# Kernel optimization log

Measured on AMD Instinct MI355X. Metric: run time of the kernel, lower is better.

## Reference

```python
import jax, jax.numpy as jnp
import numpy as np

B, N, D, H, DH, FF, CI, K, MPE = 8, 1024, 512, 8, 64, 2048, 1024, 31, 512
PAD = (K // 2, K // 2 - (K + 1) % 2)  # (15, 15)


def _ln(x, g, b):
    m = x.mean(-1, keepdims=True)
    v = ((x - m) ** 2).mean(-1, keepdims=True)
    return (x - m) * jax.lax.rsqrt(v + 1e-5) * g + b


def _swish(x):
    return x * jax.nn.sigmoid(x)


def setup_inputs() -> dict:
    key = jax.random.key(0)
    ks = iter(jax.random.split(key, 40))
    def w(shape, s=0.02):
        return (jax.random.normal(next(ks), shape) * s).astype(jnp.float32)
    ones = lambda n: jnp.ones((n,), jnp.float32)
    zeros = lambda n: jnp.zeros((n,), jnp.float32)
    return dict(
        x=jax.random.normal(next(ks), (B, N, D), dtype=jnp.float32),
        f1_g=ones(D), f1_b=zeros(D), f1_w1=w((D, FF)), f1_b1=zeros(FF), f1_w2=w((FF, D)), f1_b2=zeros(D),
        a_g=ones(D), a_b=zeros(D), wq=w((D, H * DH)), wkv=w((D, 2 * H * DH)), wo=w((H * DH, D)), wo_b=zeros(D),
        rel=w((2 * MPE + 1, DH)),
        c_g=ones(D), c_b=zeros(D), cw1=w((D, 2 * CI)), cb1=zeros(2 * CI), dw=w((CI, K)), db=zeros(CI),
        bn_g=ones(CI), bn_b=zeros(CI), bn_m=zeros(CI), bn_v=ones(CI), cw2=w((CI, D)), cb2=zeros(D),
        f2_g=ones(D), f2_b=zeros(D), f2_w1=w((D, FF)), f2_b1=zeros(FF), f2_w2=w((FF, D)), f2_b2=zeros(D),
        p_g=ones(D), p_b=zeros(D),
    )


def reference(x, f1_g, f1_b, f1_w1, f1_b1, f1_w2, f1_b2,
              a_g, a_b, wq, wkv, wo, wo_b, rel,
              c_g, c_b, cw1, cb1, dw, db, bn_g, bn_b, bn_m, bn_v, cw2, cb2,
              f2_g, f2_b, f2_w1, f2_b1, f2_w2, f2_b2, p_g, p_b):
    # FF1 (half-step)
    h = _ln(x, f1_g, f1_b)
    x = x + 0.5 * (_swish(h @ f1_w1 + f1_b1) @ f1_w2 + f1_b2)
    # Attention with relative positional bias
    h = _ln(x, a_g, a_b)
    q = (h @ wq).reshape(B, N, H, DH).transpose(0, 2, 1, 3)          # bhnd
    k, v = jnp.split(h @ wkv, 2, axis=-1)
    k = k.reshape(B, N, H, DH).transpose(0, 2, 1, 3)
    v = v.reshape(B, N, H, DH).transpose(0, 2, 1, 3)
    scale = DH ** -0.5
    dots = jnp.einsum('bhid,bhjd->bhij', q, k) * scale
    seq = jnp.arange(N)
    dist = jnp.clip(seq[:, None] - seq[None, :], -MPE, MPE) + MPE    # [N,N]
    rp = rel[dist]                                                   # [N,N,DH]
    dots = dots + jnp.einsum('bhnd,nrd->bhnr', q, rp) * scale
    attn = jax.nn.softmax(dots, axis=-1)
    o = jnp.einsum('bhij,bhjd->bhid', attn, v).transpose(0, 2, 1, 3).reshape(B, N, H * DH)
    x = x + o @ wo + wo_b
    # Conv module: LN -> pw conv -> GLU -> depthwise conv -> BN(eval) -> swish -> pw conv
    h = _ln(x, c_g, c_b)
    h = h @ cw1 + cb1                                                # [B,N,2CI]
    out, gate = jnp.split(h, 2, axis=-1)
    h = (out * jax.nn.sigmoid(gate)).transpose(0, 2, 1)              # [B,CI,N]
    h = jnp.pad(h, ((0, 0), (0, 0), PAD))
    h = jax.lax.conv_general_dilated(h, dw[:, None, :], (1,), 'VALID',
                                     feature_group_count=CI,
                                     dimension_numbers=('NCH', 'OIH', 'NCH')) + db[None, :, None]
    h = (h - bn_m[None, :, None]) * jax.lax.rsqrt(bn_v[None, :, None] + 1e-5) * bn_g[None, :, None] + bn_b[None, :, None]
    h = _swish(h).transpose(0, 2, 1)                                 # [B,N,CI]
    x = x + h @ cw2 + cb2
    # FF2 (half-step) + post norm
    h = _ln(x, f2_g, f2_b)
    x = x + 0.5 * (_swish(h @ f2_w1 + f2_b1) @ f2_w2 + f2_b2)
    return _ln(x, p_g, p_b)
```

## Files before the change

kernel.cpp:

```cpp
#include <hip/hip_runtime.h>
#include <hip/hip_bf16.h>
#include <cstdint>


using bf16_t = __hip_bfloat16;
typedef __bf16 bf16x8 __attribute__((ext_vector_type(8)));
typedef float floatx4 __attribute__((ext_vector_type(4)));

struct alignas(16) hbf8 { bf16_t h[8]; };
struct alignas(8)  hbf4 { bf16_t h[4]; };

__device__ __forceinline__ float  b2f(bf16_t h) { return __bfloat162float(h); }
__device__ __forceinline__ bf16_t f2b(float f)  { return __float2bfloat16(f); }
__device__ __forceinline__ float  sig_(float x) { return 1.f / (1.f + __expf(-x)); }

__device__ __forceinline__ void async16(const void* g, void* l) {
  __builtin_amdgcn_global_load_lds(
      (const __attribute__((address_space(1))) unsigned int*)(uintptr_t)g,
      (__attribute__((address_space(3))) unsigned int*)(uintptr_t)l, 16, 0, 0);
}

struct GemmArgs {
  const bf16_t* A; const bf16_t* Bt; const float* bias; const float* srcf;
  bf16_t* C; float* resid;
  int K, lda, ldb, ldc;
  long sAb, sAh, sBb, sBh, sCb, sCh;
  float alpha, beta;
};

template <int BM, int BN, int WR, int WC, int EPI>
__global__ __launch_bounds__(256) void gemm_bt(GemmArgs g) {
  constexpr int FM = BM / (WR * 16);
  constexpr int FN = BN / (WC * 16);
  constexpr int IA = (BM * 4) / 256;
  constexpr int IB = (BN * 4) / 256;
  __shared__ __align__(16) bf16_t As[BM * 32];
  __shared__ __align__(16) bf16_t Bs[BN * 32];
  const int tid = threadIdx.x;
  const int lane = tid & 63, w = tid >> 6;
  int bx = blockIdx.x, by = blockIdx.y;
  {
    const int gx = gridDim.x;
    const int nwg = gx * gridDim.y;
    if ((nwg & 7) == 0 && gridDim.z == 1) {
      int lin = by * gx + bx;
      int lid = (lin & 7) * (nwg >> 3) + (lin >> 3);
      bx = lid % gx; by = lid / gx;
    }
  }
  const int bm0 = by * BM, bn0 = bx * BN;
  const int zb = blockIdx.z >> 3, zh = blockIdx.z & 7;
  const bf16_t* Ab = g.A + (long)zb * g.sAb + (long)zh * g.sAh;
  const bf16_t* Bb = g.Bt + (long)zb * g.sBb + (long)zh * g.sBh;
  const int wm0 = (w / WC) * (FM * 16);
  const int wn0 = (w % WC) * (FN * 16);
  const int lrow = lane & 15, lq = lane >> 4;

  floatx4 acc[FM][FN] = {};

  for (int k0 = 0; k0 < g.K; k0 += 32) {
#pragma unroll
    for (int i = 0; i < IA; ++i) {
      int c = i * 256 + tid;
      int m = c >> 2, kk = (c & 3) * 8;
      async16(Ab + (long)(bm0 + m) * g.lda + (k0 + kk), (char*)As + c * 16);
    }
#pragma unroll
    for (int i = 0; i < IB; ++i) {
      int c = i * 256 + tid;
      int n = bn0 + (c >> 2), kk = (c & 3) * 8;
      async16(Bb + (long)n * g.ldb + (k0 + kk), (char*)Bs + c * 16);
    }
    __syncthreads();
    bf16x8 af[FM], bfr[FN];
#pragma unroll
    for (int fm = 0; fm < FM; ++fm)
      af[fm] = *(const bf16x8*)(As + (wm0 + fm * 16 + lrow) * 32 + lq * 8);
#pragma unroll
    for (int fn = 0; fn < FN; ++fn)
      bfr[fn] = *(const bf16x8*)(Bs + (wn0 + fn * 16 + lrow) * 32 + lq * 8);
#pragma unroll
    for (int fm = 0; fm < FM; ++fm)
#pragma unroll
      for (int fn = 0; fn < FN; ++fn)
        acc[fm][fn] = __builtin_amdgcn_mfma_f32_16x16x32_bf16(af[fm], bfr[fn], acc[fm][fn], 0, 0, 0);
    __syncthreads();
  }

  const int bi = bm0 + wm0 + lq * 4;
  const int bj = bn0 + wn0 + lrow;
  if constexpr (EPI == 2) {
    float* R = g.resid;
    const float* S = g.srcf;
#pragma unroll
    for (int fm = 0; fm < FM; ++fm)
#pragma unroll
      for (int fn = 0; fn < FN; ++fn) {
        int j = bj + fn * 16;
        float bv = g.bias ? g.bias[j] : 0.f;
#pragma unroll
        for (int r = 0; r < 4; ++r) {
          long i = bi + fm * 16 + r;
          float base = S ? S[i * g.ldc + j] : R[i * g.ldc + j];
          R[i * g.ldc + j] = base + g.beta * (acc[fm][fn][r] + bv);
        }
      }
  } else if constexpr (EPI == 4) {
    bf16_t* C = g.C;
#pragma unroll
    for (int fm = 0; fm < FM; ++fm)
#pragma unroll
      for (int fn = 0; fn < FN; ++fn) {
        int j = bj + fn * 16;
        float bv = g.bias[(j >> 1) + (j & 1) * 1024];
#pragma unroll
        for (int r = 0; r < 4; ++r) {
          int i = bi + fm * 16 + r;
          float v = acc[fm][fn][r] + bv;
          float gp = __shfl_xor(v, 1);
          if ((j & 1) == 0)
            C[(long)i * g.ldc + (j >> 1)] = f2b(v * sig_(gp));
        }
      }
  } else {
    bf16_t* C = g.C + (long)zb * g.sCb + (long)zh * g.sCh;
#pragma unroll
    for (int fm = 0; fm < FM; ++fm)
#pragma unroll
      for (int fn = 0; fn < FN; ++fn) {
        int j = bj + fn * 16;
        float bv = g.bias ? g.bias[j] : 0.f;
#pragma unroll
        for (int r = 0; r < 4; ++r) {
          int i = bi + fm * 16 + r;
          float v = acc[fm][fn][r];
          if constexpr (EPI == 0) v = g.alpha * v + bv;
          if constexpr (EPI == 1) { v += bv; v = v * sig_(v); }
          C[(long)i * g.ldc + j] = f2b(v);
        }
      }
  }
}

__global__ __launch_bounds__(512, 4) void attn_kernel(
    const bf16_t* __restrict__ QKV, const bf16_t* __restrict__ VT,
    const bf16_t* __restrict__ RELP, bf16_t* __restrict__ O) {
  constexpr int LDT = 1028;
  __shared__ __align__(16) bf16_t Tls[32 * LDT];
  __shared__ float scr[576];

  const int tid = threadIdx.x;
  const int w = tid >> 6, lane = tid & 63;
  const int lrow = lane & 15, lq = lane >> 4;
  const int lin = blockIdx.y * gridDim.x + blockIdx.x;
  const int lid = (lin & 7) * 256 + (lin >> 3);
  const int z = lid >> 5;
  const int i0 = (lid & 31) * 32;
  const int b = z >> 3, zh = z & 7;
  const int j0w = w * 128;

  const bf16_t* Qb  = QKV + ((long)(b * 1024 + i0)) * 1536 + zh * 64;
  const bf16_t* Kb  = QKV + ((long)b * 1024) * 1536 + 512 + zh * 64;
  const bf16_t* VTb = VT + ((long)(b * 8 + zh)) * 65536;

  bf16x8 af[2][2];
#pragma unroll
  for (int fm = 0; fm < 2; ++fm)
#pragma unroll
    for (int ks = 0; ks < 2; ++ks)
      af[fm][ks] = *(const bf16x8*)(Qb + (long)(fm * 16 + lrow) * 1536 + ks * 32 + lq * 8);

  {
    const int u0w = w * 144;
    bf16x8 rf[18];
#pragma unroll
    for (int fnT = 0; fnT < 9; ++fnT) {
      const int u0 = u0w + fnT * 16;
      if (u0 < LDT) {
        rf[2 * fnT]     = *(const bf16x8*)(RELP + (long)(u0 + lrow) * 64 + lq * 8);
        rf[2 * fnT + 1] = *(const bf16x8*)(RELP + (long)(u0 + lrow) * 64 + 32 + lq * 8);
      }
    }
#pragma unroll
    for (int fnT = 0; fnT < 9; ++fnT) {
      const int u0 = u0w + fnT * 16;
      if (u0 < LDT) {
        floatx4 tacc[2] = {};
        tacc[0] = __builtin_amdgcn_mfma_f32_16x16x32_bf16(af[0][0], rf[2 * fnT],     tacc[0], 0, 0, 0);
        tacc[0] = __builtin_amdgcn_mfma_f32_16x16x32_bf16(af[0][1], rf[2 * fnT + 1], tacc[0], 0, 0, 0);
        tacc[1] = __builtin_amdgcn_mfma_f32_16x16x32_bf16(af[1][0], rf[2 * fnT],     tacc[1], 0, 0, 0);
        tacc[1] = __builtin_amdgcn_mfma_f32_16x16x32_bf16(af[1][1], rf[2 * fnT + 1], tacc[1], 0, 0, 0);
        const int uu = u0 + lrow;
#pragma unroll
        for (int fm = 0; fm < 2; ++fm)
#pragma unroll
          for (int r = 0; r < 4; ++r)
            if (uu < LDT)
              Tls[(fm * 16 + lq * 4 + r) * LDT + uu] = f2b(tacc[fm][r]);
      }
    }
  }

  bf16x8 kfA[8], kfB[8];
#pragma unroll
  for (int x = 0; x < 8; ++x)
    kfA[x] = *(const bf16x8*)(Kb + (long)(j0w + (x >> 1) * 16 + lrow) * 1536 + (x & 1) * 32 + lq * 8);
#pragma unroll
  for (int x = 0; x < 8; ++x)
    kfB[x] = *(const bf16x8*)(Kb + (long)(j0w + (4 + (x >> 1)) * 16 + lrow) * 1536 + (x & 1) * 32 + lq * 8);
  __syncthreads();

  floatx4 sacc[2][8] = {};
#pragma unroll
  for (int fn = 0; fn < 4; ++fn) {
    sacc[0][fn] = __builtin_amdgcn_mfma_f32_16x16x32_bf16(af[0][0], kfA[2 * fn],     sacc[0][fn], 0, 0, 0);
    sacc[0][fn] = __builtin_amdgcn_mfma_f32_16x16x32_bf16(af[0][1], kfA[2 * fn + 1], sacc[0][fn], 0, 0, 0);
    sacc[1][fn] = __builtin_amdgcn_mfma_f32_16x16x32_bf16(af[1][0], kfA[2 * fn],     sacc[1][fn], 0, 0, 0);
    sacc[1][fn] = __builtin_amdgcn_mfma_f32_16x16x32_bf16(af[1][1], kfA[2 * fn + 1], sacc[1][fn], 0, 0, 0);
  }
#pragma unroll
  for (int fn = 4; fn < 8; ++fn) {
    sacc[0][fn] = __builtin_amdgcn_mfma_f32_16x16x32_bf16(af[0][0], kfB[2 * (fn - 4)],     sacc[0][fn], 0, 0, 0);
    sacc[0][fn] = __builtin_amdgcn_mfma_f32_16x16x32_bf16(af[0][1], kfB[2 * (fn - 4) + 1], sacc[0][fn], 0, 0, 0);
    sacc[1][fn] = __builtin_amdgcn_mfma_f32_16x16x32_bf16(af[1][0], kfB[2 * (fn - 4)],     sacc[1][fn], 0, 0, 0);
    sacc[1][fn] = __builtin_amdgcn_mfma_f32_16x16x32_bf16(af[1][1], kfB[2 * (fn - 4) + 1], sacc[1][fn], 0, 0, 0);
  }

#pragma unroll
  for (int fm = 0; fm < 2; ++fm)
#pragma unroll
    for (int r = 0; r < 4; ++r) {
      const int il = fm * 16 + lq * 4 + r;
      const bf16_t* trow = Tls + il * LDT + 512;
      const int tb = i0 + il - j0w - lrow;
#pragma unroll
      for (int fn = 0; fn < 8; ++fn) {
        int t = tb - fn * 16;
        t = t < -512 ? -512 : (t > 512 ? 512 : t);
        sacc[fm][fn][r] += b2f(trow[t]);
      }
    }

  float rmax[2][4];
#pragma unroll
  for (int fm = 0; fm < 2; ++fm)
#pragma unroll
    for (int r = 0; r < 4; ++r) {
      float m = sacc[fm][0][r];
#pragma unroll
      for (int fn = 1; fn < 8; ++fn) m = fmaxf(m, sacc[fm][fn][r]);
      rmax[fm][r] = m;
    }
#pragma unroll
  for (int off = 1; off < 16; off <<= 1)
#pragma unroll
    for (int fm = 0; fm < 2; ++fm)
#pragma unroll
      for (int r = 0; r < 4; ++r)
        rmax[fm][r] = fmaxf(rmax[fm][r], __shfl_xor(rmax[fm][r], off));
  if (lrow == 0)
#pragma unroll
    for (int fm = 0; fm < 2; ++fm)
#pragma unroll
      for (int r = 0; r < 4; ++r)
        scr[(fm * 16 + lq * 4 + r) * 9 + w] = rmax[fm][r];

  float rsum[2][4];
#pragma unroll
  for (int fm = 0; fm < 2; ++fm)
#pragma unroll
    for (int r = 0; r < 4; ++r) {
      float s = 0.f;
#pragma unroll
      for (int fn = 0; fn < 8; ++fn) {
        float e = __expf(sacc[fm][fn][r] - rmax[fm][r]);
        sacc[fm][fn][r] = e;
        s += e;
      }
      rsum[fm][r] = s;
    }
#pragma unroll
  for (int off = 1; off < 16; off <<= 1)
#pragma unroll
    for (int fm = 0; fm < 2; ++fm)
#pragma unroll
      for (int r = 0; r < 4; ++r)
        rsum[fm][r] += __shfl_xor(rsum[fm][r], off);
  if (lrow == 0)
#pragma unroll
    for (int fm = 0; fm < 2; ++fm)
#pragma unroll
      for (int r = 0; r < 4; ++r)
        scr[288 + (fm * 16 + lq * 4 + r) * 9 + w] = rsum[fm][r];

  bf16x8 vfA[8];
#pragma unroll
  for (int x = 0; x < 8; ++x)
    vfA[x] = *(const bf16x8*)(VTb + (long)((x & 3) * 16 + lrow) * 1024 + j0w + (x >> 2) * 32 + lq * 8);

  __syncthreads();

#pragma unroll
  for (int fm = 0; fm < 2; ++fm)
#pragma unroll
    for (int fn = 0; fn < 8; ++fn)
#pragma unroll
      for (int r = 0; r < 4; ++r) {
        const int i = fm * 16 + lq * 4 + r;
        const int j = j0w + fn * 16 + lrow;
        const unsigned boff = (unsigned)(i * 2048 + j * 2) ^ ((unsigned)(i & 7) << 4);
        *(bf16_t*)((char*)Tls + boff) = f2b(sacc[fm][fn][r]);
      }

  bf16x8 vfB[8];
#pragma unroll
  for (int x = 0; x < 8; ++x)
    vfB[x] = *(const bf16x8*)(VTb + (long)((x & 3) * 16 + lrow) * 1024 + j0w + 64 + (x >> 2) * 32 + lq * 8);

  floatx4 oacc[2][4] = {};
#pragma unroll
  for (int ks = 0; ks < 4; ++ks) {
    const int j = j0w + ks * 32;
    bf16x8 ap[2];
#pragma unroll
    for (int fm = 0; fm < 2; ++fm) {
      const int i = fm * 16 + lrow;
      const unsigned boff = (unsigned)(i * 2048 + (j + lq * 8) * 2) ^ ((unsigned)(i & 7) << 4);
      ap[fm] = *(const bf16x8*)((char*)Tls + boff);
    }
#pragma unroll
    for (int fd = 0; fd < 4; ++fd) {
      bf16x8 bv = (ks < 2) ? vfA[(ks << 2) | fd] : vfB[((ks - 2) << 2) | fd];
      oacc[0][fd] = __builtin_amdgcn_mfma_f32_16x16x32_bf16(ap[0], bv, oacc[0][fd], 0, 0, 0);
      oacc[1][fd] = __builtin_amdgcn_mfma_f32_16x16x32_bf16(ap[1], bv, oacc[1][fd], 0, 0, 0);
    }
  }
  __syncthreads();

  {
    float* part = (float*)Tls + w * 2048;
#pragma unroll
    for (int fm = 0; fm < 2; ++fm)
#pragma unroll
      for (int fd = 0; fd < 4; ++fd)
#pragma unroll
        for (int r = 0; r < 4; ++r)
          part[(fm * 16 + lq * 4 + r) * 64 + fd * 16 + lrow] = oacc[fm][fd][r];
  }
  __syncthreads();

  {
    const int i = tid >> 4;
    const int d0 = (tid & 15) * 4;
    float mw[8], sw[8];
#pragma unroll
    for (int ww = 0; ww < 8; ++ww) {
      mw[ww] = scr[i * 9 + ww];
      sw[ww] = scr[288 + i * 9 + ww];
    }
    float M = mw[0];
#pragma unroll
    for (int ww = 1; ww < 8; ++ww) M = fmaxf(M, mw[ww]);
    float fac[8]; float tot = 0.f;
#pragma unroll
    for (int ww = 0; ww < 8; ++ww) { fac[ww] = __expf(mw[ww] - M); tot += sw[ww] * fac[ww]; }
    const float inv = 1.f / tot;
    floatx4 s = {};
#pragma unroll
    for (int ww = 0; ww < 8; ++ww) {
      floatx4 p = *(const floatx4*)((const float*)Tls + ww * 2048 + i * 64 + d0);
      s += p * fac[ww];
    }
    hbf4 o4;
#pragma unroll
    for (int m = 0; m < 4; ++m) o4.h[m] = f2b(s[m] * inv);
    *(hbf4*)(O + (long)(b * 1024 + i0 + i) * 512 + zh * 64 + d0) = o4;
  }
}

__global__ __launch_bounds__(256) void diag_kernel(float* __restrict__ out, long n, float v) {
  long i = (long)blockIdx.x * 256 + threadIdx.x;
  if (i < n) out[i] = v;
}

struct PrepJobs {
  const float* src[10];
  bf16_t*      dst[10];
  int R[10], C[10], gx[10], start[10];
  float scale[10];
  int   mode[10];
  int   njobs;
};

__global__ __launch_bounds__(256) void prep_kernel(PrepJobs P) {
  __shared__ float t[32][33];
  const int bid = blockIdx.x;
  int j = 0;
  while (j + 1 < P.njobs && bid >= P.start[j + 1]) ++j;
  const int tile = bid - P.start[j];
  const int tid = threadIdx.x;
  if (P.mode[j] == 2) {
    int i = tile * 256 + tid;
    if (i < 73728) {
      int r = i >> 6, c = i & 63;
      P.dst[j][i] = (r < 1025) ? f2b(P.src[j][r * 64 + c]) : f2b(0.f);
    }
    return;
  }
  const int gx = P.gx[j];
  const int c0 = (tile % gx) * 32, r0 = (tile / gx) * 32;
  const int C = P.C[j], R = P.R[j];
  const float scale = P.scale[j];
  const int tx = tid & 31, ty = tid >> 5;
#pragma unroll
  for (int i = 0; i < 4; ++i)
    t[ty + i * 8][tx] = P.src[j][(long)(r0 + ty + i * 8) * C + c0 + tx];
  __syncthreads();
#pragma unroll
  for (int i = 0; i < 4; ++i) {
    int c = c0 + ty + i * 8;
    int row = (P.mode[j] == 1) ? ((c < 1024) ? 2 * c : 2 * (c - 1024) + 1) : c;
    P.dst[j][(long)row * R + r0 + tx] = f2b(t[tx][ty + i * 8] * scale);
  }
}

template <bool F32OUT>
__global__ __launch_bounds__(256) void ln_kernel(const float* __restrict__ X, const float* __restrict__ gam,
                                                 const float* __restrict__ bet, void* __restrict__ outv) {
  int row = blockIdx.x, tid = threadIdx.x;
  const float* x = X + (long)row * 512;
  float a = x[tid], b = x[tid + 256];
  float s = a + b, q = a * a + b * b;
  for (int off = 32; off; off >>= 1) { s += __shfl_down(s, off); q += __shfl_down(q, off); }
  __shared__ float red[8];
  int w = tid >> 6;
  if ((tid & 63) == 0) { red[w] = s; red[w + 4] = q; }
  __syncthreads();
  float ts = red[0] + red[1] + red[2] + red[3];
  float tq = red[4] + red[5] + red[6] + red[7];
  float mean = ts * (1.f / 512.f);
  float var = tq * (1.f / 512.f) - mean * mean;
  float rs = rsqrtf(var + 1e-5f);
  float o0 = (a - mean) * rs * gam[tid]       + bet[tid];
  float o1 = (b - mean) * rs * gam[tid + 256] + bet[tid + 256];
  if constexpr (F32OUT) {
    float* out = (float*)outv;
    out[(long)row * 512 + tid]       = o0;
    out[(long)row * 512 + tid + 256] = o1;
  } else {
    bf16_t* out = (bf16_t*)outv;
    out[(long)row * 512 + tid]       = f2b(o0);
    out[(long)row * 512 + tid + 256] = f2b(o1);
  }
}

__global__ __launch_bounds__(256) void vt_kernel(const bf16_t* __restrict__ QKV, bf16_t* __restrict__ VT) {
  int jb = blockIdx.x, z = blockIdx.y;
  int b = z >> 3, h = z & 7;
  const bf16_t* src = QKV + (long)b * 1024 * 1536 + 1024 + h * 64;
  bf16_t* dst = VT + (long)z * 65536;
  __shared__ bf16_t t[64][65];
  int tid = threadIdx.x;
#pragma unroll
  for (int i = 0; i < 16; ++i) {
    int l = i * 256 + tid;
    int j = l >> 6, d = l & 63;
    t[d][j] = src[(long)(jb * 64 + j) * 1536 + d];
  }
  __syncthreads();
#pragma unroll
  for (int i = 0; i < 16; ++i) {
    int l = i * 256 + tid;
    int d = l >> 6, j = l & 63;
    dst[(long)d * 1024 + jb * 64 + j] = t[d][j];
  }
}

__global__ __launch_bounds__(256) void dwconv_kernel(const bf16_t* __restrict__ G, const float* __restrict__ dw,
    const float* __restrict__ db, const float* __restrict__ bng, const float* __restrict__ bnb,
    const float* __restrict__ bnm, const float* __restrict__ bnv, bf16_t* __restrict__ out) {
  int n0 = blockIdx.x * 32, c0 = blockIdx.y * 64, b = blockIdx.z;
  __shared__ bf16_t t[62][64];
  __shared__ float dws[31][64];
  int tid = threadIdx.x;
  const bf16_t* src = G + (long)b * 1024 * 1024 + c0;
#pragma unroll
  for (int i = 0; i < 16; ++i) {
    int l = i * 256 + tid;
    if (l < 3968) {
      int rr = l >> 6, c = l & 63;
      int n = n0 - 15 + rr;
      t[rr][c] = (n >= 0 && n < 1024) ? src[(long)n * 1024 + c] : f2b(0.f);
    }
  }
#pragma unroll
  for (int i = 0; i < 8; ++i) {
    int l = i * 256 + tid;
    if (l < 1984) {
      int k = l >> 6, c = l & 63;
      dws[k][c] = dw[(long)(c0 + c) * 31 + k];
    }
  }
  __syncthreads();
  int c = tid & 63, nl = tid >> 6;
  float rs = rsqrtf(bnv[c0 + c] + 1e-5f);
  float sc = rs * bng[c0 + c];
  float ab = (db[c0 + c] - bnm[c0 + c]) * sc + bnb[c0 + c];
#pragma unroll
  for (int j = 0; j < 8; ++j) {
    int rr = nl * 8 + j;
    float s = 0.f;
#pragma unroll
    for (int k = 0; k < 31; ++k) s += b2f(t[rr + k][c]) * dws[k][c];
    float y = s * sc + ab;
    out[((long)b * 1024 + n0 + rr) * 1024 + c0 + c] = f2b(y * sig_(y));
  }
}

extern "C" void kernel_launch(void* const* d_in, const int* in_sizes, int n_in,
                              void* d_out, int out_size, void* d_ws, size_t ws_size,
                              hipStream_t stream) {
  auto fail = [&](float code) {
    diag_kernel<<<(out_size + 255) / 256, 256, 0, stream>>>((float*)d_out, out_size, code);
  };
  if (n_in != 34)             { fail(70.f);  return; }
  if (in_sizes[0] != 4194304) { fail(80.f);  return; }

  const float* x     = (const float*)d_in[0];
  const float* f1_g  = (const float*)d_in[1];
  const float* f1_b  = (const float*)d_in[2];
  const float* f1_w1 = (const float*)d_in[3];
  const float* f1_b1 = (const float*)d_in[4];
  const float* f1_w2 = (const float*)d_in[5];
  const float* f1_b2 = (const float*)d_in[6];
  const float* a_g   = (const float*)d_in[7];
  const float* a_b   = (const float*)d_in[8];
  const float* wq    = (const float*)d_in[9];
  const float* wkv   = (const float*)d_in[10];
  const float* wo    = (const float*)d_in[11];
  const float* wo_b  = (const float*)d_in[12];
  const float* rel   = (const float*)d_in[13];
  const float* c_g   = (const float*)d_in[14];
  const float* c_b   = (const float*)d_in[15];
  const float* cw1   = (const float*)d_in[16];
  const float* cb1   = (const float*)d_in[17];
  const float* dwp   = (const float*)d_in[18];
  const float* dbp   = (const float*)d_in[19];
  const float* bn_g  = (const float*)d_in[20];
  const float* bn_b  = (const float*)d_in[21];
  const float* bn_m  = (const float*)d_in[22];
  const float* bn_v  = (const float*)d_in[23];
  const float* cw2   = (const float*)d_in[24];
  const float* cb2   = (const float*)d_in[25];
  const float* f2_g  = (const float*)d_in[26];
  const float* f2_b  = (const float*)d_in[27];
  const float* f2_w1 = (const float*)d_in[28];
  const float* f2_b1 = (const float*)d_in[29];
  const float* f2_w2 = (const float*)d_in[30];
  const float* f2_b2 = (const float*)d_in[31];
  const float* p_g   = (const float*)d_in[32];
  const float* p_b   = (const float*)d_in[33];

  char* ws = (char*)d_ws;
  const size_t OFF_X  = 0;
  const size_t OFF_WT = 16777216;
  const size_t OFF_D  = 30408704;
  const size_t OFF_E  = 63963136;
  const size_t relp_off = OFF_E + 33554432;
  if (ws_size < relp_off + 147456ULL) { fail(200.f); return; }

  float*  X   = (float*)(ws + OFF_X);
  bf16_t* WT  = (bf16_t*)(ws + OFF_WT);
  bf16_t* QKV = (bf16_t*)(ws + OFF_D);
  bf16_t* VT  = (bf16_t*)(ws + OFF_D + 25165824);
  bf16_t* GLU = (bf16_t*)(ws + OFF_D);
  bf16_t* DWO = (bf16_t*)(ws + OFF_D + 16777216);
  bf16_t* MID = (bf16_t*)(ws + OFF_E);
  bf16_t* RELP= (bf16_t*)(ws + relp_off);
  bf16_t* H   = (bf16_t*)d_out;
  bf16_t* O   = (bf16_t*)d_out;

  bf16_t* f1_w1t = WT;            bf16_t* f1_w2t = WT + 1048576;
  bf16_t* wqkvt  = WT + 2097152;
  bf16_t* wot    = WT + 2883584;  bf16_t* cw1t   = WT + 3145728;
  bf16_t* cw2t   = WT + 4194304;  bf16_t* f2_w1t = WT + 4718592;
  bf16_t* f2_w2t = WT + 5767168;

  auto GA = [](const bf16_t* A, const bf16_t* Bt, const float* bias, bf16_t* C,
               float* resid, const float* srcf, int K, int lda, int ldb, int ldc,
               float alpha, float beta) {
    GemmArgs g{}; g.A = A; g.Bt = Bt; g.bias = bias; g.srcf = srcf; g.C = C; g.resid = resid;
    g.K = K; g.lda = lda; g.ldb = ldb; g.ldc = ldc;
    g.sAb = g.sAh = g.sBb = g.sBh = g.sCb = g.sCh = 0; g.alpha = alpha; g.beta = beta;
    return g;
  };

  {
    PrepJobs P{};
    auto set = [&](int idx, const float* s, bf16_t* d, int R, int C, int start,
                   float sc, int mode) {
      P.src[idx] = s; P.dst[idx] = d; P.R[idx] = R; P.C[idx] = C;
      P.gx[idx] = C / 32; P.start[idx] = start; P.scale[idx] = sc; P.mode[idx] = mode;
    };
    set(0, f1_w1, f1_w1t,          512, 2048,    0, 1.f,    0);
    set(1, f1_w2, f1_w2t,         2048,  512, 1024, 1.f,    0);
    set(2, wq,    wqkvt,           512,  512, 2048, 0.125f, 0);
    set(3, wkv,   wqkvt + 262144,  512, 1024, 2304, 1.f,    0);
    set(4, wo,    wot,             512,  512, 2816, 1.f,    0);
    set(5, cw1,   cw1t,            512, 2048, 3072, 1.f,    1);
    set(6, cw2,   cw2t,           1024,  512, 4096, 1.f,    0);
    set(7, f2_w1, f2_w1t,          512, 2048, 4608, 1.f,    0);
    set(8, f2_w2, f2_w2t,         2048,  512, 5632, 1.f,    0);
    set(9, rel,   RELP,           1025,   64, 6656, 1.f,    2);
    P.njobs = 10;
    prep_kernel<<<6944, 256, 0, stream>>>(P);
  }

  ln_kernel<false><<<8192, 256, 0, stream>>>(x, f1_g, f1_b, H);
  { GemmArgs g = GA(H, f1_w1t, f1_b1, MID, nullptr, nullptr, 512, 512, 512, 2048, 1.f, 0.f);
    gemm_bt<128, 128, 2, 2, 1><<<dim3(16, 64, 1), 256, 0, stream>>>(g); }
  { GemmArgs g = GA(MID, f1_w2t, f1_b2, nullptr, X, x, 2048, 2048, 2048, 512, 1.f, 0.5f);
    gemm_bt<64, 128, 1, 4, 2><<<dim3(4, 128, 1), 256, 0, stream>>>(g); }

  ln_kernel<false><<<8192, 256, 0, stream>>>(X, a_g, a_b, H);
  { GemmArgs g = GA(H, wqkvt, nullptr, QKV, nullptr, nullptr, 512, 512, 512, 1536, 1.f, 0.f);
    gemm_bt<128, 128, 2, 2, 0><<<dim3(12, 64, 1), 256, 0, stream>>>(g); }
  vt_kernel<<<dim3(16, 64), 256, 0, stream>>>(QKV, VT);

  attn_kernel<<<dim3(32, 64), 512, 0, stream>>>(QKV, VT, RELP, O);

  { GemmArgs g = GA(O, wot, wo_b, nullptr, X, nullptr, 512, 512, 512, 512, 1.f, 1.f);
    gemm_bt<64, 128, 1, 4, 2><<<dim3(4, 128, 1), 256, 0, stream>>>(g); }

  ln_kernel<false><<<8192, 256, 0, stream>>>(X, c_g, c_b, H);
  { GemmArgs g = GA(H, cw1t, cb1, GLU, nullptr, nullptr, 512, 512, 512, 1024, 1.f, 0.f);
    gemm_bt<128, 128, 2, 2, 4><<<dim3(16, 64, 1), 256, 0, stream>>>(g); }
  dwconv_kernel<<<dim3(32, 16, 8), 256, 0, stream>>>(GLU, dwp, dbp, bn_g, bn_b, bn_m, bn_v, DWO);
  { GemmArgs g = GA(DWO, cw2t, cb2, nullptr, X, nullptr, 1024, 1024, 1024, 512, 1.f, 1.f);
    gemm_bt<64, 128, 1, 4, 2><<<dim3(4, 128, 1), 256, 0, stream>>>(g); }

  ln_kernel<false><<<8192, 256, 0, stream>>>(X, f2_g, f2_b, H);
  { GemmArgs g = GA(H, f2_w1t, f2_b1, MID, nullptr, nullptr, 512, 512, 512, 2048, 1.f, 0.f);
    gemm_bt<128, 128, 2, 2, 1><<<dim3(16, 64, 1), 256, 0, stream>>>(g); }
  { GemmArgs g = GA(MID, f2_w2t, f2_b2, nullptr, X, nullptr, 2048, 2048, 2048, 512, 1.f, 0.5f);
    gemm_bt<64, 128, 1, 4, 2><<<dim3(4, 128, 1), 256, 0, stream>>>(g); }
  ln_kernel<true><<<8192, 256, 0, stream>>>(X, p_g, p_b, (float*)d_out);
}
```

Measured before the change: 625.6 us.

## Double GEMM K-tile, transpose rel-pos MFMA for packed stores, vectorize dwconv loads

The GEMM K step grows from 32 to 64, which halves the number of barrier pairs per K loop at the cost of twice the LDS tile size. In attention, the relative-position product is computed with the operands swapped so each lane writes 4 contiguous packed bf16 values instead of scattered scalar stores. The tail guard changes and now depends on LDT. The depthwise conv staging loads 16-byte vectors instead of single bf16 elements.

```diff
diff --git a/kernel.cpp b/kernel.cpp
--- a/kernel.cpp
+++ b/kernel.cpp
@@ -13,6 +13,14 @@
 __device__ __forceinline__ float  b2f(bf16_t h) { return __bfloat162float(h); }
 __device__ __forceinline__ bf16_t f2b(float f)  { return __float2bfloat16(f); }
 __device__ __forceinline__ float  sig_(float x) { return 1.f / (1.f + __expf(-x)); }
+
+__device__ __forceinline__ unsigned pkbf(float a, float b) {
+  bf16_t ha = f2b(a), hb = f2b(b);
+  unsigned short ua, ub;
+  __builtin_memcpy(&ua, &ha, 2);
+  __builtin_memcpy(&ub, &hb, 2);
+  return (unsigned)ua | ((unsigned)ub << 16);
+}
 
 __device__ __forceinline__ void async16(const void* g, void* l) {
   __builtin_amdgcn_global_load_lds(
@@ -32,10 +40,10 @@
 __global__ __launch_bounds__(256) void gemm_bt(GemmArgs g) {
   constexpr int FM = BM / (WR * 16);
   constexpr int FN = BN / (WC * 16);
-  constexpr int IA = (BM * 4) / 256;
-  constexpr int IB = (BN * 4) / 256;
-  __shared__ __align__(16) bf16_t As[BM * 32];
-  __shared__ __align__(16) bf16_t Bs[BN * 32];
+  constexpr int IA = BM / 32;
+  constexpr int IB = BN / 32;
+  __shared__ __align__(16) bf16_t As[BM * 64];
+  __shared__ __align__(16) bf16_t Bs[BN * 64];
   const int tid = threadIdx.x;
   const int lane = tid & 63, w = tid >> 6;
   int bx = blockIdx.x, by = blockIdx.y;
@@ -58,32 +66,35 @@
 
   floatx4 acc[FM][FN] = {};
 
-  for (int k0 = 0; k0 < g.K; k0 += 32) {
+  for (int k0 = 0; k0 < g.K; k0 += 64) {
 #pragma unroll
     for (int i = 0; i < IA; ++i) {
       int c = i * 256 + tid;
-      int m = c >> 2, kk = (c & 3) * 8;
+      int m = c >> 3, kk = (c & 7) * 8;
       async16(Ab + (long)(bm0 + m) * g.lda + (k0 + kk), (char*)As + c * 16);
     }
 #pragma unroll
     for (int i = 0; i < IB; ++i) {
       int c = i * 256 + tid;
-      int n = bn0 + (c >> 2), kk = (c & 3) * 8;
+      int n = bn0 + (c >> 3), kk = (c & 7) * 8;
       async16(Bb + (long)n * g.ldb + (k0 + kk), (char*)Bs + c * 16);
     }
     __syncthreads();
-    bf16x8 af[FM], bfr[FN];
-#pragma unroll
-    for (int fm = 0; fm < FM; ++fm)
-      af[fm] = *(const bf16x8*)(As + (wm0 + fm * 16 + lrow) * 32 + lq * 8);
-#pragma unroll
-    for (int fn = 0; fn < FN; ++fn)
-      bfr[fn] = *(const bf16x8*)(Bs + (wn0 + fn * 16 + lrow) * 32 + lq * 8);
-#pragma unroll
-    for (int fm = 0; fm < FM; ++fm)
+#pragma unroll
+    for (int ks = 0; ks < 2; ++ks) {
+      bf16x8 af[FM], bfr[FN];
+#pragma unroll
+      for (int fm = 0; fm < FM; ++fm)
+        af[fm] = *(const bf16x8*)(As + (wm0 + fm * 16 + lrow) * 64 + ks * 32 + lq * 8);
 #pragma unroll
       for (int fn = 0; fn < FN; ++fn)
-        acc[fm][fn] = __builtin_amdgcn_mfma_f32_16x16x32_bf16(af[fm], bfr[fn], acc[fm][fn], 0, 0, 0);
+        bfr[fn] = *(const bf16x8*)(Bs + (wn0 + fn * 16 + lrow) * 64 + ks * 32 + lq * 8);
+#pragma unroll
+      for (int fm = 0; fm < FM; ++fm)
+#pragma unroll
+        for (int fn = 0; fn < FN; ++fn)
+          acc[fm][fn] = __builtin_amdgcn_mfma_f32_16x16x32_bf16(af[fm], bfr[fn], acc[fm][fn], 0, 0, 0);
+    }
     __syncthreads();
   }
 
@@ -176,7 +187,7 @@
 #pragma unroll
     for (int fnT = 0; fnT < 9; ++fnT) {
       const int u0 = u0w + fnT * 16;
-      if (u0 < LDT) {
+      if (u0 <= 1024) {
         rf[2 * fnT]     = *(const bf16x8*)(RELP + (long)(u0 + lrow) * 64 + lq * 8);
         rf[2 * fnT + 1] = *(const bf16x8*)(RELP + (long)(u0 + lrow) * 64 + 32 + lq * 8);
       }
@@ -184,19 +195,17 @@
 #pragma unroll
     for (int fnT = 0; fnT < 9; ++fnT) {
       const int u0 = u0w + fnT * 16;
-      if (u0 < LDT) {
-        floatx4 tacc[2] = {};
-        tacc[0] = __builtin_amdgcn_mfma_f32_16x16x32_bf16(af[0][0], rf[2 * fnT],     tacc[0], 0, 0, 0);
-        tacc[0] = __builtin_amdgcn_mfma_f32_16x16x32_bf16(af[0][1], rf[2 * fnT + 1], tacc[0], 0, 0, 0);
-        tacc[1] = __builtin_amdgcn_mfma_f32_16x16x32_bf16(af[1][0], rf[2 * fnT],     tacc[1], 0, 0, 0);
-        tacc[1] = __builtin_amdgcn_mfma_f32_16x16x32_bf16(af[1][1], rf[2 * fnT + 1], tacc[1], 0, 0, 0);
-        const int uu = u0 + lrow;
-#pragma unroll
-        for (int fm = 0; fm < 2; ++fm)
-#pragma unroll
-          for (int r = 0; r < 4; ++r)
-            if (uu < LDT)
-              Tls[(fm * 16 + lq * 4 + r) * LDT + uu] = f2b(tacc[fm][r]);
+      if (u0 <= 1024) {
+#pragma unroll
+        for (int fm = 0; fm < 2; ++fm) {
+          floatx4 t4 = {};
+          t4 = __builtin_amdgcn_mfma_f32_16x16x32_bf16(rf[2 * fnT],     af[fm][0], t4, 0, 0, 0);
+          t4 = __builtin_amdgcn_mfma_f32_16x16x32_bf16(rf[2 * fnT + 1], af[fm][1], t4, 0, 0, 0);
+          if (u0 + lq * 4 + 4 <= LDT) {
+            uint2 v; v.x = pkbf(t4[0], t4[1]); v.y = pkbf(t4[2], t4[3]);
+            *(uint2*)(Tls + (long)(fm * 16 + lrow) * LDT + u0 + lq * 4) = v;
+          }
+        }
       }
     }
   }
@@ -485,12 +494,15 @@
   int tid = threadIdx.x;
   const bf16_t* src = G + (long)b * 1024 * 1024 + c0;
 #pragma unroll
-  for (int i = 0; i < 16; ++i) {
+  for (int i = 0; i < 2; ++i) {
     int l = i * 256 + tid;
-    if (l < 3968) {
-      int rr = l >> 6, c = l & 63;
+    if (l < 496) {
+      int rr = l >> 3, c8 = (l & 7) * 8;
       int n = n0 - 15 + rr;
-      t[rr][c] = (n >= 0 && n < 1024) ? src[(long)n * 1024 + c] : f2b(0.f);
+      hbf8 v;
+      if (n >= 0 && n < 1024) v = *(const hbf8*)(src + (long)n * 1024 + c8);
+      else { for (int m = 0; m < 8; ++m) v.h[m] = f2b(0.f); }
+      *(hbf8*)&t[rr][c8] = v;
     }
   }
 #pragma unroll
```

Measured after the change: 632.3 us. No clear change (+1.1%).
